# Optimization experiments

Hardware: AMD Instinct MI355X
Metric: run time of the kernel (lower is better)

Reference implementation:

```python
import jax, jax.numpy as jnp
import numpy as np

D = 1024      # input_dim
H = 1024      # expert_hidden_dim
O = 1024      # output_dim
E = 8         # num_experts
TOPK = 2
B, N_OBJ = 4, 4096


def setup_inputs() -> dict:
    key = jax.random.key(0)
    ks = jax.random.split(key, 7)
    s_in = 1.0 / np.sqrt(D)
    s_h = 1.0 / np.sqrt(H)
    return {
        "x":  jax.random.normal(ks[0], (B, N_OBJ, D), dtype=jnp.float32),
        "Wr": jax.random.uniform(ks[1], (D, E), jnp.float32, -s_in, s_in),
        "br": jax.random.uniform(ks[2], (E,), jnp.float32, -s_in, s_in),
        "W1": jax.random.uniform(ks[3], (E, D, H), jnp.float32, -s_in, s_in),
        "b1": jax.random.uniform(ks[4], (E, H), jnp.float32, -s_in, s_in),
        "W2": jax.random.uniform(ks[5], (E, H, O), jnp.float32, -s_h, s_h),
        "b2": jax.random.uniform(ks[6], (E, O), jnp.float32, -s_h, s_h),
    }


def reference(x, Wr, br, W1, b1, W2, b2):
    # Router: (B, N, E)
    logits = jnp.einsum("bnd,de->bne", x, Wr) + br
    # sparse top-k routing: softmax over the top-k logits only
    topv, topi = jax.lax.top_k(logits, TOPK)          # (B, N, k)
    coef = jax.nn.softmax(topv, axis=-1)              # (B, N, k)
    # scatter per-expert coefficients into dense (B, N, E); zeros for non-selected
    coef_full = jnp.sum(
        jax.nn.one_hot(topi, E, dtype=x.dtype) * coef[..., None], axis=-2
    )                                                 # (B, N, E)
    # All-expert dense compute (as in original module; dropout is eval-mode identity)
    h = jax.nn.relu(jnp.einsum("bnd,edh->benh", x, W1) + b1[:, None, :])  # (B,E,N,H)
    y = jnp.einsum("benh,eho->beno", h, W2) + b2[:, None, :]              # (B,E,N,O)
    # Weighted combine over experts
    out = jnp.einsum("beno,bne->bno", y, coef_full)                        # (B,N,O)
    return out
```

## Files before the change

kernel.cpp:

```cpp
#include <hip/hip_runtime.h>
#include <cstdint>

typedef unsigned short u16;
using bf16x8 = __attribute__((ext_vector_type(8))) __bf16;
using f32x4  = __attribute__((ext_vector_type(4))) float;
typedef u16 u16x8 __attribute__((ext_vector_type(8)));

#define T_TOK 16384
#define E_NUM 8

__device__ __forceinline__ u16 f2bf(float f) {
    union { float f; unsigned u; } v; v.f = f;
    unsigned r = (v.u + 0x7FFFu + ((v.u >> 16) & 1u)) >> 16;
    return (u16)r;
}

__device__ __forceinline__ void gload_lds16(const void* g, void* l) {
    __builtin_amdgcn_global_load_lds(
        (const __attribute__((address_space(1))) void*)g,
        (__attribute__((address_space(3))) void*)l, 16, 0, 0);
}

__global__ __launch_bounds__(256) void k_transpose(const float* __restrict__ W, u16* __restrict__ WT) {
    __shared__ float tile[32][33];
    int e = blockIdx.z;
    int d0 = blockIdx.x << 5, h0 = blockIdx.y << 5;
    int tx = threadIdx.x & 31, ty = threadIdx.x >> 5;
    const size_t eo = (size_t)e << 20;
#pragma unroll
    for (int i = 0; i < 4; ++i) {
        int r = ty + i * 8;
        tile[r][tx] = W[eo + (size_t)(d0 + r) * 1024 + h0 + tx];
    }
    __syncthreads();
#pragma unroll
    for (int i = 0; i < 4; ++i) {
        int r = ty + i * 8;
        WT[eo + (size_t)(h0 + r) * 1024 + d0 + tx] = f2bf(tile[tx][r]);
    }
}

__global__ __launch_bounds__(256) void k_router(const float* __restrict__ x, const float* __restrict__ Wr,
                                                const float* __restrict__ br,
                                                int* __restrict__ tinfo, float* __restrict__ c1arr,
                                                u16* __restrict__ xbf) {
    const int wave = threadIdx.x >> 6, lane = threadIdx.x & 63;
    const int t = (blockIdx.x << 2) + wave;
    const float* xr = x + (size_t)t * 1024;
    u16* xbr = xbf + (size_t)t * 1024;
    float acc[8] = {0, 0, 0, 0, 0, 0, 0, 0};
#pragma unroll
    for (int i = 0; i < 16; ++i) {
        int d = (i << 6) + lane;
        float xv = xr[d];
        xbr[d] = f2bf(xv);
        float4 w0 = *(const float4*)(Wr + d * 8);
        float4 w1 = *(const float4*)(Wr + d * 8 + 4);
        acc[0] += xv * w0.x; acc[1] += xv * w0.y; acc[2] += xv * w0.z; acc[3] += xv * w0.w;
        acc[4] += xv * w1.x; acc[5] += xv * w1.y; acc[6] += xv * w1.z; acc[7] += xv * w1.w;
    }
#pragma unroll
    for (int off = 32; off > 0; off >>= 1)
#pragma unroll
        for (int e = 0; e < 8; ++e) acc[e] += __shfl_xor(acc[e], off);

    if (lane == 0) {
        float v1 = -1e30f, v2 = -1e30f; int i1 = 0, i2 = 0;
#pragma unroll
        for (int e = 0; e < 8; ++e) {
            float v = acc[e] + br[e];
            if (v > v1) { v2 = v1; i2 = i1; v1 = v; i1 = e; }
            else if (v > v2) { v2 = v; i2 = e; }
        }
        float c1 = 1.f / (1.f + expf(v2 - v1));
        tinfo[t] = i1 | (i2 << 4);
        c1arr[t] = c1;
    }
}

__global__ __launch_bounds__(1024) void k_scatter(const int* __restrict__ tinfo, const float* __restrict__ c1arr,
                                                  int* __restrict__ cnt, int* __restrict__ tok,
                                                  float* __restrict__ coef) {
    __shared__ int lcnt[8];
    __shared__ int lbase[8];
    const int tid = threadIdx.x;
    const int t = blockIdx.x * 1024 + tid;
    if (tid < 8) lcnt[tid] = 0;
    __syncthreads();
    int info = tinfo[t];
    float c1 = c1arr[t];
    int g1 = info & 15;
    int g2 = (info >> 4) & 15;
    int o1 = atomicAdd(&lcnt[g1], 1);
    int o2 = atomicAdd(&lcnt[g2], 1);
    __syncthreads();
    if (tid < 8) lbase[tid] = atomicAdd(cnt + tid, lcnt[tid]);
    __syncthreads();
    int p1 = lbase[g1] + o1;
    tok[(g1 << 14) + p1] = t; coef[(g1 << 14) + p1] = c1;
    int p2 = lbase[g2] + o2;
    tok[(g2 << 14) + p2] = t; coef[(g2 << 14) + p2] = 1.f - c1;
}

template <int PHASE>
__global__ __launch_bounds__(256, 3) void k_gemm(
    const int* __restrict__ cnt, const int* __restrict__ tok, const float* __restrict__ coef,
    const u16* __restrict__ xbf, const u16* __restrict__ w1t, const u16* __restrict__ w2t,
    const float* __restrict__ b1, const float* __restrict__ b2,
    u16* __restrict__ hbuf, float* __restrict__ out)
{
    __shared__ u16 a_s[128 * 64];
    __shared__ u16 b_s[128 * 64];
    __shared__ int s_cnt[8];
    __shared__ int tok_s[128];
    __shared__ float coef_s[128];

    const int tid = threadIdx.x;
    if (tid < 8) s_cnt[tid] = cnt[tid];
    __syncthreads();

    int bid = blockIdx.x + blockIdx.y * 264;
    int lin = (bid & 7) * 264 + (bid >> 3);
    int xt = lin >> 3, yt = lin & 7;

    int g = -1, tile = 0, r0 = 0, mt = xt, rb = 0;
    for (int gg = 0; gg < 8; ++gg) {
        int c = s_cnt[gg], tg = (c + 127) >> 7;
        if (g < 0) {
            if (mt < tg) { g = gg; tile = mt; r0 = rb + (mt << 7); }
            else mt -= tg;
        }
        rb += c;
    }
    if (g < 0) return;
    const int cntg = s_cnt[g];
    const int e = g;
    const int nb = yt << 7;
    const int rowlim = cntg - (tile << 7);

    if (tid < 128) {
        int idx = (tile << 7) + tid;
        bool valid = idx < cntg;
        tok_s[tid] = valid ? tok[(g << 14) + idx] : 0;
        coef_s[tid] = valid ? coef[(g << 14) + idx] : 0.f;
    }
    __syncthreads();

    const int w = tid >> 6, l = tid & 63;
    const int wrow = (w >> 1) << 6, wcol = (w & 1) << 6;
    const u16* asrc = (PHASE == 0) ? xbf : hbuf;
    const u16* bsrc = (PHASE == 0) ? w1t : w2t;
    const size_t brow0 = ((size_t)e << 10) + nb;

    const int sw = ((l & 7) ^ (l >> 3)) << 3;
    const int xk = (l & 7) << 3;

    const u16* aptr[4]; int ldsa[4];
#pragma unroll
    for (int j = 0; j < 4; ++j) {
        int row = (j << 5) + (w << 3) + (l >> 3);
        int arow = (PHASE == 0) ? tok_s[row] : (r0 + row);
        aptr[j] = asrc + ((size_t)arow << 10) + sw;
        ldsa[j] = ((j << 5) + (w << 3)) * 64;
    }
    const u16* bptr[4]; int ldsb[4];
#pragma unroll
    for (int j = 0; j < 4; ++j) {
        int brow = (j << 5) + (w << 3) + (l >> 3);
        bptr[j] = bsrc + (brow0 + brow) * 1024 + sw;
        ldsb[j] = ((j << 5) + (w << 3)) * 64;
    }

    f32x4 acc[4][4];
#pragma unroll
    for (int mi = 0; mi < 4; ++mi)
#pragma unroll
        for (int ni = 0; ni < 4; ++ni) { acc[mi][ni][0] = 0.f; acc[mi][ni][1] = 0.f; acc[mi][ni][2] = 0.f; acc[mi][ni][3] = 0.f; }

    for (int kc = 0; kc < 16; ++kc) {
        const int ko = kc << 6;
#pragma unroll
        for (int j = 0; j < 4; ++j) gload_lds16(aptr[j] + ko, &a_s[ldsa[j]]);
#pragma unroll
        for (int j = 0; j < 4; ++j) gload_lds16(bptr[j] + ko, &b_s[ldsb[j]]);
        __syncthreads();
#pragma unroll
        for (int ks = 0; ks < 64; ks += 32) {
            const int co = (ks + ((l >> 4) << 3)) ^ xk;
            bf16x8 af[4], bfr[4];
#pragma unroll
            for (int mi = 0; mi < 4; ++mi)
                af[mi] = *(const bf16x8*)&a_s[(wrow + (mi << 4) + (l & 15)) * 64 + co];
#pragma unroll
            for (int ni = 0; ni < 4; ++ni)
                bfr[ni] = *(const bf16x8*)&b_s[(wcol + (ni << 4) + (l & 15)) * 64 + co];
#pragma unroll
            for (int mi = 0; mi < 4; ++mi)
#pragma unroll
                for (int ni = 0; ni < 4; ++ni)
                    acc[mi][ni] = __builtin_amdgcn_mfma_f32_16x16x32_bf16(af[mi], bfr[ni], acc[mi][ni], 0, 0, 0);
        }
        __syncthreads();
    }

    const int rq = (l >> 4) << 2;
    const int cl = l & 15;
#pragma unroll
    for (int ni = 0; ni < 4; ++ni) {
        int ccol = wcol + (ni << 4) + cl;
        float bias = (PHASE == 0 ? b1 : b2)[((size_t)e << 10) + nb + ccol];
#pragma unroll
        for (int mi = 0; mi < 4; ++mi) {
            int rbase = wrow + (mi << 4) + rq;
#pragma unroll
            for (int j = 0; j < 4; ++j) {
                int r = rbase + j;
                if (r < rowlim) {
                    float v = acc[mi][ni][j] + bias;
                    if constexpr (PHASE == 0) {
                        v = fmaxf(v, 0.f);
                        hbuf[(size_t)(r0 + r) * 1024 + nb + ccol] = f2bf(v);
                    } else {
                        atomicAdd(out + ((size_t)tok_s[r] << 10) + nb + ccol, v * coef_s[r]);
                    }
                }
            }
        }
    }
}

__global__ __launch_bounds__(256) void k_naive(const float* __restrict__ x, const float* __restrict__ Wr,
    const float* __restrict__ br, const float* __restrict__ W1, const float* __restrict__ b1,
    const float* __restrict__ W2, const float* __restrict__ b2, float* __restrict__ out)
{
    __shared__ float xs[1024];
    __shared__ float hs[1024];
    __shared__ float red[4];
    __shared__ float lg[8];
    const int tid = threadIdx.x;
    const size_t t = blockIdx.x;
    for (int i = tid; i < 1024; i += 256) xs[i] = x[t * 1024 + i];
    __syncthreads();
    float lacc[8] = {0, 0, 0, 0, 0, 0, 0, 0};
    for (int d = tid; d < 1024; d += 256) {
        float xv = xs[d];
#pragma unroll
        for (int e = 0; e < 8; ++e) lacc[e] += xv * Wr[d * 8 + e];
    }
    for (int e = 0; e < 8; ++e) {
        float v = lacc[e];
        for (int off = 32; off > 0; off >>= 1) v += __shfl_xor(v, off);
        if ((tid & 63) == 0) red[tid >> 6] = v;
        __syncthreads();
        if (tid == 0) lg[e] = red[0] + red[1] + red[2] + red[3] + br[e];
        __syncthreads();
    }
    float v1 = -1e30f, v2 = -1e30f; int i1 = 0, i2 = 0;
    for (int e = 0; e < 8; ++e) {
        float v = lg[e];
        if (v > v1) { v2 = v1; i2 = i1; v1 = v; i1 = e; }
        else if (v > v2) { v2 = v; i2 = e; }
    }
    float c1 = 1.f / (1.f + expf(v2 - v1)), c2 = 1.f - c1;
    float yacc[4] = {0, 0, 0, 0};
    for (int slot = 0; slot < 2; ++slot) {
        int e = slot ? i2 : i1;
        float cw = slot ? c2 : c1;
        __syncthreads();
        float ha[4];
        for (int jb = 0; jb < 4; ++jb) {
            int j = (jb << 8) + tid;
            float a = b1[(e << 10) + j];
            for (int d = 0; d < 1024; ++d) a += xs[d] * W1[(((size_t)e << 10) + d) * 1024 + j];
            ha[jb] = fmaxf(a, 0.f);
        }
        for (int jb = 0; jb < 4; ++jb) hs[(jb << 8) + tid] = ha[jb];
        __syncthreads();
        for (int ob = 0; ob < 4; ++ob) {
            int o = (ob << 8) + tid;
            float a = b2[(e << 10) + o];
            for (int h = 0; h < 1024; ++h) a += hs[h] * W2[(((size_t)e << 10) + h) * 1024 + o];
            yacc[ob] += cw * a;
        }
    }
    for (int ob = 0; ob < 4; ++ob) out[t * 1024 + (ob << 8) + tid] = yacc[ob];
}

extern "C" void kernel_launch(void* const* d_in, const int* in_sizes, int n_in,
                              void* d_out, int out_size, void* d_ws, size_t ws_size,
                              hipStream_t stream) {
    const float* x  = (const float*)d_in[0];
    const float* Wr = (const float*)d_in[1];
    const float* br = (const float*)d_in[2];
    const float* W1 = (const float*)d_in[3];
    const float* b1 = (const float*)d_in[4];
    const float* W2 = (const float*)d_in[5];
    const float* b2 = (const float*)d_in[6];
    float* out = (float*)d_out;

    const size_t OFF_TOK   = (size_t)1 << 20;
    const size_t OFF_COEF  = (size_t)2 << 20;
    const size_t OFF_TINFO = (size_t)3 << 20;
    const size_t OFF_C1    = OFF_TINFO + (size_t)T_TOK * 4;
    const size_t OFF_XBF   = (size_t)4 << 20;
    const size_t OFF_W1T   = OFF_XBF + (size_t)T_TOK * 1024 * 2;
    const size_t OFF_W2T   = OFF_W1T + (size_t)E_NUM * 1024 * 1024 * 2;
    const size_t OFF_H     = OFF_W2T + (size_t)E_NUM * 1024 * 1024 * 2;
    const size_t WS_NEED   = OFF_H + (size_t)(2 * T_TOK + 128) * 1024 * 2;

    if (ws_size < WS_NEED) {
        k_naive<<<T_TOK, 256, 0, stream>>>(x, Wr, br, W1, b1, W2, b2, out);
        return;
    }

    char* ws = (char*)d_ws;
    int*   cnt   = (int*)ws;
    int*   tok   = (int*)(ws + OFF_TOK);
    float* coef  = (float*)(ws + OFF_COEF);
    int*   tinfo = (int*)(ws + OFF_TINFO);
    float* c1arr = (float*)(ws + OFF_C1);
    u16*   xbf   = (u16*)(ws + OFF_XBF);
    u16*   w1t   = (u16*)(ws + OFF_W1T);
    u16*   w2t   = (u16*)(ws + OFF_W2T);
    u16*   hbuf  = (u16*)(ws + OFF_H);

    hipMemsetAsync(cnt, 0, 64, stream);
    hipMemsetAsync(d_out, 0, (size_t)out_size * sizeof(float), stream);
    k_transpose<<<dim3(32, 32, 8), 256, 0, stream>>>(W1, w1t);
    k_transpose<<<dim3(32, 32, 8), 256, 0, stream>>>(W2, w2t);
    k_router<<<4096, 256, 0, stream>>>(x, Wr, br, tinfo, c1arr, xbf);
    k_scatter<<<16, 1024, 0, stream>>>(tinfo, c1arr, cnt, tok, coef);
    dim3 gg(264, 8);
    k_gemm<0><<<gg, 256, 0, stream>>>(cnt, tok, coef, xbf, w1t, w2t, b1, b2, hbuf, out);
    k_gemm<1><<<gg, 256, 0, stream>>>(cnt, tok, coef, xbf, w1t, w2t, b1, b2, hbuf, out);
}
```

Baseline: 370.9 us.

## Enlarge expert GEMM tiles to 256x256 with double-buffered LDS prefetch

The expert GEMM tile grows from 128x128 to 256x256, using 512 threads per block and 8x4 MFMA accumulators per wave. This roughly halves global and LDS traffic per FLOP. The LDS buffers are also double-buffered so the next K-chunk's global-to-LDS load is issued before computing the current one, with one barrier per iteration instead of two. The cost is about 128KB of LDS and many more accumulator registers per block, so occupancy is likely one block per CU. The coarser grid of 544 blocks may also leave an unbalanced tail wave.

```diff
diff --git a/kernel.cpp b/kernel.cpp
--- a/kernel.cpp
+++ b/kernel.cpp
@@ -103,31 +103,31 @@
 }
 
 template <int PHASE>
-__global__ __launch_bounds__(256, 3) void k_gemm(
+__global__ __launch_bounds__(512, 2) void k_gemm(
     const int* __restrict__ cnt, const int* __restrict__ tok, const float* __restrict__ coef,
     const u16* __restrict__ xbf, const u16* __restrict__ w1t, const u16* __restrict__ w2t,
     const float* __restrict__ b1, const float* __restrict__ b2,
     u16* __restrict__ hbuf, float* __restrict__ out)
 {
-    __shared__ u16 a_s[128 * 64];
-    __shared__ u16 b_s[128 * 64];
+    __shared__ u16 a_s[2][256 * 64];
+    __shared__ u16 b_s[2][256 * 64];
     __shared__ int s_cnt[8];
-    __shared__ int tok_s[128];
-    __shared__ float coef_s[128];
+    __shared__ int tok_s[256];
+    __shared__ float coef_s[256];
 
     const int tid = threadIdx.x;
     if (tid < 8) s_cnt[tid] = cnt[tid];
     __syncthreads();
 
-    int bid = blockIdx.x + blockIdx.y * 264;
-    int lin = (bid & 7) * 264 + (bid >> 3);
-    int xt = lin >> 3, yt = lin & 7;
+    int bid = blockIdx.x + blockIdx.y * 68;
+    int lin = (bid & 7) * 68 + (bid >> 3);
+    int xt = lin >> 2, yt = lin & 3;
 
     int g = -1, tile = 0, r0 = 0, mt = xt, rb = 0;
     for (int gg = 0; gg < 8; ++gg) {
-        int c = s_cnt[gg], tg = (c + 127) >> 7;
+        int c = s_cnt[gg], tg = (c + 255) >> 8;
         if (g < 0) {
-            if (mt < tg) { g = gg; tile = mt; r0 = rb + (mt << 7); }
+            if (mt < tg) { g = gg; tile = mt; r0 = rb + (mt << 8); }
             else mt -= tg;
         }
         rb += c;
@@ -135,11 +135,11 @@
     if (g < 0) return;
     const int cntg = s_cnt[g];
     const int e = g;
-    const int nb = yt << 7;
-    const int rowlim = cntg - (tile << 7);
-
-    if (tid < 128) {
-        int idx = (tile << 7) + tid;
+    const int nb = yt << 8;
+    const int rowlim = cntg - (tile << 8);
+
+    if (tid < 256) {
+        int idx = (tile << 8) + tid;
         bool valid = idx < cntg;
         tok_s[tid] = valid ? tok[(g << 14) + idx] : 0;
         coef_s[tid] = valid ? coef[(g << 14) + idx] : 0.f;
@@ -147,7 +147,8 @@
     __syncthreads();
 
     const int w = tid >> 6, l = tid & 63;
-    const int wrow = (w >> 1) << 6, wcol = (w & 1) << 6;
+    const int wrow = (w >> 2) << 7;
+    const int wcol = (w & 3) << 6;
     const u16* asrc = (PHASE == 0) ? xbf : hbuf;
     const u16* bsrc = (PHASE == 0) ? w1t : w2t;
     const size_t brow0 = ((size_t)e << 10) + nb;
@@ -158,50 +159,62 @@
     const u16* aptr[4]; int ldsa[4];
 #pragma unroll
     for (int j = 0; j < 4; ++j) {
-        int row = (j << 5) + (w << 3) + (l >> 3);
+        int row = (j << 6) + (w << 3) + (l >> 3);
         int arow = (PHASE == 0) ? tok_s[row] : (r0 + row);
         aptr[j] = asrc + ((size_t)arow << 10) + sw;
-        ldsa[j] = ((j << 5) + (w << 3)) * 64;
+        ldsa[j] = ((j << 6) + (w << 3)) * 64;
     }
     const u16* bptr[4]; int ldsb[4];
 #pragma unroll
     for (int j = 0; j < 4; ++j) {
-        int brow = (j << 5) + (w << 3) + (l >> 3);
+        int brow = (j << 6) + (w << 3) + (l >> 3);
         bptr[j] = bsrc + (brow0 + brow) * 1024 + sw;
-        ldsb[j] = ((j << 5) + (w << 3)) * 64;
-    }
-
-    f32x4 acc[4][4];
-#pragma unroll
-    for (int mi = 0; mi < 4; ++mi)
+        ldsb[j] = ((j << 6) + (w << 3)) * 64;
+    }
+
+    f32x4 acc[8][4];
+#pragma unroll
+    for (int mi = 0; mi < 8; ++mi)
 #pragma unroll
         for (int ni = 0; ni < 4; ++ni) { acc[mi][ni][0] = 0.f; acc[mi][ni][1] = 0.f; acc[mi][ni][2] = 0.f; acc[mi][ni][3] = 0.f; }
 
+#define STAGE(BUF, KO)                                                  \
+    {                                                                   \
+        _Pragma("unroll")                                               \
+        for (int j = 0; j < 4; ++j) gload_lds16(aptr[j] + (KO), &a_s[BUF][ldsa[j]]); \
+        _Pragma("unroll")                                               \
+        for (int j = 0; j < 4; ++j) gload_lds16(bptr[j] + (KO), &b_s[BUF][ldsb[j]]); \
+    }
+
+    STAGE(0, 0);
+    __syncthreads();
+
+    int cur = 0;
     for (int kc = 0; kc < 16; ++kc) {
-        const int ko = kc << 6;
-#pragma unroll
-        for (int j = 0; j < 4; ++j) gload_lds16(aptr[j] + ko, &a_s[ldsa[j]]);
-#pragma unroll
-        for (int j = 0; j < 4; ++j) gload_lds16(bptr[j] + ko, &b_s[ldsb[j]]);
-        __syncthreads();
+        if (kc < 15) {
+            const int ko = (kc + 1) << 6;
+            if (cur == 0) STAGE(1, ko) else STAGE(0, ko);
+        }
 #pragma unroll
         for (int ks = 0; ks < 64; ks += 32) {
             const int co = (ks + ((l >> 4) << 3)) ^ xk;
-            bf16x8 af[4], bfr[4];
-#pragma unroll
-            for (int mi = 0; mi < 4; ++mi)
-                af[mi] = *(const bf16x8*)&a_s[(wrow + (mi << 4) + (l & 15)) * 64 + co];
+            bf16x8 af[8], bfr[4];
+#pragma unroll
+            for (int mi = 0; mi < 8; ++mi)
+                af[mi] = *(const bf16x8*)&a_s[cur][(wrow + (mi << 4) + (l & 15)) * 64 + co];
 #pragma unroll
             for (int ni = 0; ni < 4; ++ni)
-                bfr[ni] = *(const bf16x8*)&b_s[(wcol + (ni << 4) + (l & 15)) * 64 + co];
-#pragma unroll
-            for (int mi = 0; mi < 4; ++mi)
+                bfr[ni] = *(const bf16x8*)&b_s[cur][(wcol + (ni << 4) + (l & 15)) * 64 + co];
+#pragma unroll
+            for (int mi = 0; mi < 8; ++mi)
 #pragma unroll
                 for (int ni = 0; ni < 4; ++ni)
                     acc[mi][ni] = __builtin_amdgcn_mfma_f32_16x16x32_bf16(af[mi], bfr[ni], acc[mi][ni], 0, 0, 0);
         }
         __syncthreads();
-    }
+        cur ^= 1;
+    }
+#undef STAGE
 
     const int rq = (l >> 4) << 2;
     const int cl = l & 15;
@@ -210,7 +223,7 @@
         int ccol = wcol + (ni << 4) + cl;
         float bias = (PHASE == 0 ? b1 : b2)[((size_t)e << 10) + nb + ccol];
 #pragma unroll
-        for (int mi = 0; mi < 4; ++mi) {
+        for (int mi = 0; mi < 8; ++mi) {
             int rbase = wrow + (mi << 4) + rq;
 #pragma unroll
             for (int j = 0; j < 4; ++j) {
@@ -306,7 +319,7 @@
     const size_t OFF_W1T   = OFF_XBF + (size_t)T_TOK * 1024 * 2;
     const size_t OFF_W2T   = OFF_W1T + (size_t)E_NUM * 1024 * 1024 * 2;
     const size_t OFF_H     = OFF_W2T + (size_t)E_NUM * 1024 * 1024 * 2;
-    const size_t WS_NEED   = OFF_H + (size_t)(2 * T_TOK + 128) * 1024 * 2;
+    const size_t WS_NEED   = OFF_H + (size_t)(2 * T_TOK + 512) * 1024 * 2;
 
     if (ws_size < WS_NEED) {
         k_naive<<<T_TOK, 256, 0, stream>>>(x, Wr, br, W1, b1, W2, b2, out);
@@ -330,7 +343,7 @@
     k_transpose<<<dim3(32, 32, 8), 256, 0, stream>>>(W2, w2t);
     k_router<<<4096, 256, 0, stream>>>(x, Wr, br, tinfo, c1arr, xbf);
     k_scatter<<<16, 1024, 0, stream>>>(tinfo, c1arr, cnt, tok, coef);
-    dim3 gg(264, 8);
-    k_gemm<0><<<gg, 256, 0, stream>>>(cnt, tok, coef, xbf, w1t, w2t, b1, b2, hbuf, out);
-    k_gemm<1><<<gg, 256, 0, stream>>>(cnt, tok, coef, xbf, w1t, w2t, b1, b2, hbuf, out);
-}
+    dim3 gg(68, 8);
+    k_gemm<0><<<gg, 512, 0, stream>>>(cnt, tok, coef, xbf, w1t, w2t, b1, b2, hbuf, out);
+    k_gemm<1><<<gg, 512, 0, stream>>>(cnt, tok, coef, xbf, w1t, w2t, b1, b2, hbuf, out);
+}
```

After: 469.5 us. 26.6% more time.

## Double-buffer LDS tiles in expert GEMM to overlap global loads with MFMA

Applied to the files above, without the earlier changes.

The GEMM main loop now uses two LDS buffers for the A and B tiles. The next K-chunk is issued via global_load_lds while MFMAs run on the current one, which is meant to hide global memory latency behind compute. Doubling LDS per block lowers the launch-bounds occupancy hint from 3 to 2 blocks per CU, so less latency can be hidden by running more waves. The workspace size requirement is also raised slightly, which could trigger the naive fallback if the provided workspace is too small.

```diff
diff --git a/kernel.cpp b/kernel.cpp
--- a/kernel.cpp
+++ b/kernel.cpp
@@ -103,14 +103,16 @@
 }
 
 template <int PHASE>
-__global__ __launch_bounds__(256, 3) void k_gemm(
+__global__ __launch_bounds__(256, 2) void k_gemm(
     const int* __restrict__ cnt, const int* __restrict__ tok, const float* __restrict__ coef,
     const u16* __restrict__ xbf, const u16* __restrict__ w1t, const u16* __restrict__ w2t,
     const float* __restrict__ b1, const float* __restrict__ b2,
     u16* __restrict__ hbuf, float* __restrict__ out)
 {
-    __shared__ u16 a_s[128 * 64];
-    __shared__ u16 b_s[128 * 64];
+    __shared__ u16 a0_s[128 * 64];
+    __shared__ u16 a1_s[128 * 64];
+    __shared__ u16 b0_s[128 * 64];
+    __shared__ u16 b1_s[128 * 64];
     __shared__ int s_cnt[8];
     __shared__ int tok_s[128];
     __shared__ float coef_s[128];
@@ -177,31 +179,47 @@
 #pragma unroll
         for (int ni = 0; ni < 4; ++ni) { acc[mi][ni][0] = 0.f; acc[mi][ni][1] = 0.f; acc[mi][ni][2] = 0.f; acc[mi][ni][3] = 0.f; }
 
-    for (int kc = 0; kc < 16; ++kc) {
-        const int ko = kc << 6;
-#pragma unroll
-        for (int j = 0; j < 4; ++j) gload_lds16(aptr[j] + ko, &a_s[ldsa[j]]);
-#pragma unroll
-        for (int j = 0; j < 4; ++j) gload_lds16(bptr[j] + ko, &b_s[ldsb[j]]);
-        __syncthreads();
-#pragma unroll
-        for (int ks = 0; ks < 64; ks += 32) {
-            const int co = (ks + ((l >> 4) << 3)) ^ xk;
-            bf16x8 af[4], bfr[4];
-#pragma unroll
-            for (int mi = 0; mi < 4; ++mi)
-                af[mi] = *(const bf16x8*)&a_s[(wrow + (mi << 4) + (l & 15)) * 64 + co];
-#pragma unroll
-            for (int ni = 0; ni < 4; ++ni)
-                bfr[ni] = *(const bf16x8*)&b_s[(wcol + (ni << 4) + (l & 15)) * 64 + co];
-#pragma unroll
-            for (int mi = 0; mi < 4; ++mi)
-#pragma unroll
-                for (int ni = 0; ni < 4; ++ni)
-                    acc[mi][ni] = __builtin_amdgcn_mfma_f32_16x16x32_bf16(af[mi], bfr[ni], acc[mi][ni], 0, 0, 0);
-        }
-        __syncthreads();
-    }
+#define STAGE(AS, BS, KO)                                                     \
+    {                                                                         \
+        _Pragma("unroll")                                                     \
+        for (int j = 0; j < 4; ++j) gload_lds16(aptr[j] + (KO), &AS[ldsa[j]]); \
+        _Pragma("unroll")                                                     \
+        for (int j = 0; j < 4; ++j) gload_lds16(bptr[j] + (KO), &BS[ldsb[j]]); \
+    }
+
+#define COMPUTE(AS, BS)                                                       \
+    {                                                                         \
+        _Pragma("unroll")                                                     \
+        for (int ks = 0; ks < 64; ks += 32) {                                 \
+            const int co = (ks + ((l >> 4) << 3)) ^ xk;                       \
+            bf16x8 af[4], bfr[4];                                             \
+            _Pragma("unroll")                                                 \
+            for (int mi = 0; mi < 4; ++mi)                                    \
+                af[mi] = *(const bf16x8*)&AS[(wrow + (mi << 4) + (l & 15)) * 64 + co]; \
+            _Pragma("unroll")                                                 \
+            for (int ni = 0; ni < 4; ++ni)                                    \
+                bfr[ni] = *(const bf16x8*)&BS[(wcol + (ni << 4) + (l & 15)) * 64 + co]; \
+            _Pragma("unroll")                                                 \
+            for (int mi = 0; mi < 4; ++mi)                                    \
+                _Pragma("unroll")                                             \
+                for (int ni = 0; ni < 4; ++ni)                                \
+                    acc[mi][ni] = __builtin_amdgcn_mfma_f32_16x16x32_bf16(af[mi], bfr[ni], acc[mi][ni], 0, 0, 0); \
+        }                                                                     \
+    }
+
+    STAGE(a0_s, b0_s, 0);
+    __syncthreads();
+
+    for (int kc = 0; kc < 16; kc += 2) {
+        if (kc + 1 < 16) STAGE(a1_s, b1_s, (kc + 1) << 6);
+        COMPUTE(a0_s, b0_s);
+        __syncthreads();
+        if (kc + 2 < 16) STAGE(a0_s, b0_s, (kc + 2) << 6);
+        COMPUTE(a1_s, b1_s);
+        __syncthreads();
+    }
+#undef STAGE
+#undef COMPUTE
 
     const int rq = (l >> 4) << 2;
     const int cl = l & 15;
@@ -306,7 +324,7 @@
     const size_t OFF_W1T   = OFF_XBF + (size_t)T_TOK * 1024 * 2;
     const size_t OFF_W2T   = OFF_W1T + (size_t)E_NUM * 1024 * 1024 * 2;
     const size_t OFF_H     = OFF_W2T + (size_t)E_NUM * 1024 * 1024 * 2;
-    const size_t WS_NEED   = OFF_H + (size_t)(2 * T_TOK + 128) * 1024 * 2;
+    const size_t WS_NEED   = OFF_H + (size_t)(2 * T_TOK + 512) * 1024 * 2;
 
     if (ws_size < WS_NEED) {
         k_naive<<<T_TOK, 256, 0, stream>>>(x, Wr, br, W1, b1, W2, b2, out);
```

Measured after the change: 431.1 us. 1.16x slower.

## Replace LDS-staged GEMM with direct global fragment loads and wider tiles

Applied to the files above, without the earlier changes.

The expert GEMM kernel drops shared-memory staging via global_load_lds and instead has each wave load bf16 MFMA fragments directly from global memory. The block tile widens to 128x256 with an 8x4 accumulator grid per wave, the grid halves, and occupancy hints drop to 2 blocks per CU. Token indices and coefficients are read straight from global rather than cached in LDS. This removes barriers and LDS traffic, but each wave redundantly fetches the A tile, which increases global/L2 load volume and register pressure.

```diff
diff --git a/kernel.cpp b/kernel.cpp
--- a/kernel.cpp
+++ b/kernel.cpp
@@ -4,7 +4,6 @@
 typedef unsigned short u16;
 using bf16x8 = __attribute__((ext_vector_type(8))) __bf16;
 using f32x4  = __attribute__((ext_vector_type(4))) float;
-typedef u16 u16x8 __attribute__((ext_vector_type(8)));
 
 #define T_TOK 16384
 #define E_NUM 8
@@ -13,12 +12,6 @@
     union { float f; unsigned u; } v; v.f = f;
     unsigned r = (v.u + 0x7FFFu + ((v.u >> 16) & 1u)) >> 16;
     return (u16)r;
-}
-
-__device__ __forceinline__ void gload_lds16(const void* g, void* l) {
-    __builtin_amdgcn_global_load_lds(
-        (const __attribute__((address_space(1))) void*)g,
-        (__attribute__((address_space(3))) void*)l, 16, 0, 0);
 }
 
 __global__ __launch_bounds__(256) void k_transpose(const float* __restrict__ W, u16* __restrict__ WT) {
@@ -103,115 +96,85 @@
 }
 
 template <int PHASE>
-__global__ __launch_bounds__(256, 3) void k_gemm(
+__global__ __launch_bounds__(256, 2) void k_gemm(
     const int* __restrict__ cnt, const int* __restrict__ tok, const float* __restrict__ coef,
     const u16* __restrict__ xbf, const u16* __restrict__ w1t, const u16* __restrict__ w2t,
     const float* __restrict__ b1, const float* __restrict__ b2,
     u16* __restrict__ hbuf, float* __restrict__ out)
 {
-    __shared__ u16 a_s[128 * 64];
-    __shared__ u16 b_s[128 * 64];
-    __shared__ int s_cnt[8];
-    __shared__ int tok_s[128];
-    __shared__ float coef_s[128];
-
     const int tid = threadIdx.x;
-    if (tid < 8) s_cnt[tid] = cnt[tid];
-    __syncthreads();
-
-    int bid = blockIdx.x + blockIdx.y * 264;
-    int lin = (bid & 7) * 264 + (bid >> 3);
-    int xt = lin >> 3, yt = lin & 7;
-
-    int g = -1, tile = 0, r0 = 0, mt = xt, rb = 0;
+
+    int bid = blockIdx.x + blockIdx.y * 132;
+    int lin = (bid & 7) * 132 + (bid >> 3);
+    int xt = lin >> 2, yc = lin & 3;
+
+    int g = -1, tile = 0, r0 = 0, mt = xt, rb = 0, cg = 0;
+#pragma unroll
     for (int gg = 0; gg < 8; ++gg) {
-        int c = s_cnt[gg], tg = (c + 127) >> 7;
+        int c = cnt[gg], tg = (c + 127) >> 7;
         if (g < 0) {
-            if (mt < tg) { g = gg; tile = mt; r0 = rb + (mt << 7); }
+            if (mt < tg) { g = gg; tile = mt; r0 = rb + (mt << 7); cg = c; }
             else mt -= tg;
         }
         rb += c;
     }
     if (g < 0) return;
-    const int cntg = s_cnt[g];
     const int e = g;
-    const int nb = yt << 7;
-    const int rowlim = cntg - (tile << 7);
-
-    if (tid < 128) {
-        int idx = (tile << 7) + tid;
-        bool valid = idx < cntg;
-        tok_s[tid] = valid ? tok[(g << 14) + idx] : 0;
-        coef_s[tid] = valid ? coef[(g << 14) + idx] : 0.f;
-    }
-    __syncthreads();
+    const int rowlim = cg - (tile << 7);
+    const int gbase = (g << 14) + (tile << 7);
 
     const int w = tid >> 6, l = tid & 63;
-    const int wrow = (w >> 1) << 6, wcol = (w & 1) << 6;
+    const int l15 = l & 15;
+    const int lk = (l >> 4) << 3;
     const u16* asrc = (PHASE == 0) ? xbf : hbuf;
     const u16* bsrc = (PHASE == 0) ? w1t : w2t;
-    const size_t brow0 = ((size_t)e << 10) + nb;
-
-    const int sw = ((l & 7) ^ (l >> 3)) << 3;
-    const int xk = (l & 7) << 3;
-
-    const u16* aptr[4]; int ldsa[4];
-#pragma unroll
-    for (int j = 0; j < 4; ++j) {
-        int row = (j << 5) + (w << 3) + (l >> 3);
-        int arow = (PHASE == 0) ? tok_s[row] : (r0 + row);
-        aptr[j] = asrc + ((size_t)arow << 10) + sw;
-        ldsa[j] = ((j << 5) + (w << 3)) * 64;
-    }
-    const u16* bptr[4]; int ldsb[4];
-#pragma unroll
-    for (int j = 0; j < 4; ++j) {
-        int brow = (j << 5) + (w << 3) + (l >> 3);
-        bptr[j] = bsrc + (brow0 + brow) * 1024 + sw;
-        ldsb[j] = ((j << 5) + (w << 3)) * 64;
-    }
-
-    f32x4 acc[4][4];
-#pragma unroll
-    for (int mi = 0; mi < 4; ++mi)
+    const int colq = (yc << 8) + (w << 6);
+
+    const u16* aptr[8];
+#pragma unroll
+    for (int m = 0; m < 8; ++m) {
+        int row = (m << 4) + l15;
+        int arow;
+        if (PHASE == 0) arow = (row < rowlim) ? tok[gbase + row] : 0;
+        else            arow = r0 + row;
+        aptr[m] = asrc + ((size_t)arow << 10) + lk;
+    }
+    const u16* bptr[4];
+#pragma unroll
+    for (int n = 0; n < 4; ++n) {
+        int col = colq + (n << 4) + l15;
+        bptr[n] = bsrc + (((size_t)(e << 10) + col) << 10) + lk;
+    }
+
+    f32x4 acc[8][4];
+#pragma unroll
+    for (int mi = 0; mi < 8; ++mi)
 #pragma unroll
         for (int ni = 0; ni < 4; ++ni) { acc[mi][ni][0] = 0.f; acc[mi][ni][1] = 0.f; acc[mi][ni][2] = 0.f; acc[mi][ni][3] = 0.f; }
 
-    for (int kc = 0; kc < 16; ++kc) {
-        const int ko = kc << 6;
-#pragma unroll
-        for (int j = 0; j < 4; ++j) gload_lds16(aptr[j] + ko, &a_s[ldsa[j]]);
-#pragma unroll
-        for (int j = 0; j < 4; ++j) gload_lds16(bptr[j] + ko, &b_s[ldsb[j]]);
-        __syncthreads();
-#pragma unroll
-        for (int ks = 0; ks < 64; ks += 32) {
-            const int co = (ks + ((l >> 4) << 3)) ^ xk;
-            bf16x8 af[4], bfr[4];
-#pragma unroll
-            for (int mi = 0; mi < 4; ++mi)
-                af[mi] = *(const bf16x8*)&a_s[(wrow + (mi << 4) + (l & 15)) * 64 + co];
-#pragma unroll
-            for (int ni = 0; ni < 4; ++ni)
-                bfr[ni] = *(const bf16x8*)&b_s[(wcol + (ni << 4) + (l & 15)) * 64 + co];
-#pragma unroll
-            for (int mi = 0; mi < 4; ++mi)
-#pragma unroll
-                for (int ni = 0; ni < 4; ++ni)
-                    acc[mi][ni] = __builtin_amdgcn_mfma_f32_16x16x32_bf16(af[mi], bfr[ni], acc[mi][ni], 0, 0, 0);
-        }
-        __syncthreads();
+#pragma unroll
+    for (int kc = 0; kc < 32; ++kc) {
+        const int kb = kc << 5;
+        bf16x8 bfr[4], af[8];
+#pragma unroll
+        for (int n = 0; n < 4; ++n) bfr[n] = *(const bf16x8*)(bptr[n] + kb);
+#pragma unroll
+        for (int m = 0; m < 8; ++m) af[m] = *(const bf16x8*)(aptr[m] + kb);
+#pragma unroll
+        for (int m = 0; m < 8; ++m)
+#pragma unroll
+            for (int n = 0; n < 4; ++n)
+                acc[m][n] = __builtin_amdgcn_mfma_f32_16x16x32_bf16(af[m], bfr[n], acc[m][n], 0, 0, 0);
     }
 
     const int rq = (l >> 4) << 2;
-    const int cl = l & 15;
 #pragma unroll
     for (int ni = 0; ni < 4; ++ni) {
-        int ccol = wcol + (ni << 4) + cl;
-        float bias = (PHASE == 0 ? b1 : b2)[((size_t)e << 10) + nb + ccol];
-#pragma unroll
-        for (int mi = 0; mi < 4; ++mi) {
-            int rbase = wrow + (mi << 4) + rq;
+        int ccol = colq + (ni << 4) + l15;
+        float bias = (PHASE == 0 ? b1 : b2)[((size_t)e << 10) + ccol];
+#pragma unroll
+        for (int mi = 0; mi < 8; ++mi) {
+            int rbase = (mi << 4) + rq;
 #pragma unroll
             for (int j = 0; j < 4; ++j) {
                 int r = rbase + j;
@@ -219,9 +182,10 @@
                     float v = acc[mi][ni][j] + bias;
                     if constexpr (PHASE == 0) {
                         v = fmaxf(v, 0.f);
-                        hbuf[(size_t)(r0 + r) * 1024 + nb + ccol] = f2bf(v);
+                        hbuf[(size_t)(r0 + r) * 1024 + ccol] = f2bf(v);
                     } else {
-                        atomicAdd(out + ((size_t)tok_s[r] << 10) + nb + ccol, v * coef_s[r]);
+                        int gi = gbase + r;
+                        atomicAdd(out + ((size_t)tok[gi] << 10) + ccol, v * coef[gi]);
                     }
                 }
             }
@@ -306,7 +270,7 @@
     const size_t OFF_W1T   = OFF_XBF + (size_t)T_TOK * 1024 * 2;
     const size_t OFF_W2T   = OFF_W1T + (size_t)E_NUM * 1024 * 1024 * 2;
     const size_t OFF_H     = OFF_W2T + (size_t)E_NUM * 1024 * 1024 * 2;
-    const size_t WS_NEED   = OFF_H + (size_t)(2 * T_TOK + 128) * 1024 * 2;
+    const size_t WS_NEED   = OFF_H + (size_t)(2 * T_TOK + 512) * 1024 * 2;
 
     if (ws_size < WS_NEED) {
         k_naive<<<T_TOK, 256, 0, stream>>>(x, Wr, br, W1, b1, W2, b2, out);
@@ -330,7 +294,7 @@
     k_transpose<<<dim3(32, 32, 8), 256, 0, stream>>>(W2, w2t);
     k_router<<<4096, 256, 0, stream>>>(x, Wr, br, tinfo, c1arr, xbf);
     k_scatter<<<16, 1024, 0, stream>>>(tinfo, c1arr, cnt, tok, coef);
-    dim3 gg(264, 8);
+    dim3 gg(132, 8);
     k_gemm<0><<<gg, 256, 0, stream>>>(cnt, tok, coef, xbf, w1t, w2t, b1, b2, hbuf, out);
     k_gemm<1><<<gg, 256, 0, stream>>>(cnt, tok, coef, xbf, w1t, w2t, b1, b2, hbuf, out);
 }
```

Result: slower. 780.5 us (+110.4%).
